# Kernel tuning notes

Hardware: AMD Instinct MI355X
Metric: run time of the kernel (lower is better)

## Reference

```python
import jax, jax.numpy as jnp
import numpy as np

B, C, D, L, CTX = 8, 320, 24, 77, 768
NUM_GROUPS = 32
EPS = 1e-5


def setup_inputs() -> dict:
    key = jax.random.key(0)
    ks = jax.random.split(key, 8)
    s = 0.02
    return {
        "x": jax.random.normal(ks[0], (B, C, D, D, D), jnp.float32),
        "context": jax.random.normal(ks[1], (B, L, CTX), jnp.float32),
        "Wq": jax.random.normal(ks[2], (C, C), jnp.float32) * s,
        "bq": jnp.zeros((C,), jnp.float32),
        "Wk": jax.random.normal(ks[3], (C, CTX), jnp.float32) * s,
        "bk": jnp.zeros((C,), jnp.float32),
        "Wv": jax.random.normal(ks[4], (C, CTX), jnp.float32) * s,
        "bv": jnp.zeros((C,), jnp.float32),
        "Wo": jax.random.normal(ks[5], (C, C), jnp.float32) * s,
        "bo": jnp.zeros((C,), jnp.float32),
        "gamma": jnp.ones((C,), jnp.float32),
        "beta": jnp.zeros((C,), jnp.float32),
    }


def reference(x, context, Wq, bq, Wk, bk, Wv, bv, Wo, bo, gamma, beta):
    b, c = x.shape[:2]
    spatial = x.shape[2:]
    xf = x.reshape(b, c, -1)                                # [B, C, N]
    # 1x1 Conv3d == per-position channel matmul
    q = jnp.einsum('oc,bcn->bon', Wq, xf) + bq[None, :, None]
    ctx_t = context.transpose(0, 2, 1)                      # [B, CTX, L]
    k = jnp.einsum('oc,bcl->bol', Wk, ctx_t) + bk[None, :, None]
    v = jnp.einsum('oc,bcl->bol', Wv, ctx_t) + bv[None, :, None]
    # scores [B, N, L], scaled by C^-0.5 (int(C) in the original)
    qk = jnp.einsum('bcn,bcl->bnl', q, k) * (float(c) ** -0.5)
    w = jax.nn.softmax(qk, axis=-1)
    h = jnp.einsum('bcl,bnl->bcn', v, w)                    # [B, C, N]
    h = jnp.einsum('oc,bcn->bon', Wo, h) + bo[None, :, None]
    xr = h + xf                                             # residual
    # GroupNorm over (C/G, spatial) per group
    g = NUM_GROUPS
    xg = xr.reshape(b, g, -1)
    mu = jnp.mean(xg, axis=-1, keepdims=True)
    var = jnp.var(xg, axis=-1, keepdims=True)
    xn = ((xg - mu) * jax.lax.rsqrt(var + EPS)).reshape(b, c, -1)
    xn = xn * gamma[None, :, None] + beta[None, :, None]
    out = xn * jax.nn.sigmoid(xn)                           # Swish
    return out.reshape(b, c, *spatial)
```

## Files before the change

### kernel.cpp

```cpp
#include <hip/hip_runtime.h>
#include <hip/hip_bf16.h>

#define B_ 8
#define C_ 320
#define N_ 13824
#define L_ 77
#define LP 80
#define LV 96
#define CTXD 768
#define CPG 10
#define EPS_ 1e-5f
#define SCALE_ 0.05590169943749474f
#define TROW 656

typedef __attribute__((__ext_vector_type__(4))) float f32x4;
typedef __attribute__((__ext_vector_type__(8))) short s16x8;

#define WS_ACCUM 0
#define WS_T     2048
#define WS_KST   4608
#define WS_VST   414208
#define WS_K2F   823808
#define WS_V2F   1233408
#define WS_WQT   1724928
#define WS_WO    1929728

__device__ __forceinline__ unsigned short f2bf(float f) {
  union { float f; unsigned u; } v; v.f = f;
  unsigned r = v.u + 0x7FFFu + ((v.u >> 16) & 1u);
  return (unsigned short)(r >> 16);
}
__device__ __forceinline__ float bf2f(unsigned short s) {
  union { unsigned u; float f; } v; v.u = ((unsigned)s) << 16;
  return v.f;
}
__device__ __forceinline__ s16x8 cvt8(const float* p) {
  f32x4 a = *reinterpret_cast<const f32x4*>(p);
  f32x4 b = *reinterpret_cast<const f32x4*>(p + 4);
  s16x8 r;
  r[0] = (short)f2bf(a[0]); r[1] = (short)f2bf(a[1]);
  r[2] = (short)f2bf(a[2]); r[3] = (short)f2bf(a[3]);
  r[4] = (short)f2bf(b[0]); r[5] = (short)f2bf(b[1]);
  r[6] = (short)f2bf(b[2]); r[7] = (short)f2bf(b[3]);
  return r;
}
__device__ __forceinline__ f32x4 MFMA(s16x8 a, s16x8 b, f32x4 c) {
  return __builtin_amdgcn_mfma_f32_16x16x32_bf16(a, b, c, 0, 0, 0);
}

__global__ __launch_bounds__(256) void prep_kernel(const float* __restrict__ Wq,
                                                   const float* __restrict__ Wo,
                                                   const float* __restrict__ ctx,
                                                   const float* __restrict__ Wk,
                                                   const float* __restrict__ bk,
                                                   const float* __restrict__ Wv,
                                                   const float* __restrict__ bv,
                                                   unsigned short* __restrict__ wqT,
                                                   unsigned short* __restrict__ wo_bf,
                                                   unsigned short* __restrict__ kst,
                                                   unsigned short* __restrict__ vst,
                                                   float* __restrict__ zws) {
  int bid = blockIdx.x;
  if (bid < 400) {
    int t = bid * 256 + threadIdx.x;
    if (t >= C_ * C_) return;
    int o = t / C_, c = t - o * C_;
    wqT[c * C_ + o] = f2bf(Wq[t]);
    wo_bf[t] = f2bf(Wo[t]);
    return;
  }
  int kb = bid - 400;
  { int t = kb * 256 + threadIdx.x; if (t < 1152) zws[t] = 0.f; }
  int lt = kb % 5;
  int kb5 = kb / 5;
  int b = kb5 / 5;
  int oc = kb5 % 5;
  int w = threadIdx.x >> 6, lane = threadIdx.x & 63;
  int r = lane & 15, h = lane >> 4;
  int o_row = oc * 64 + w * 16 + r;
  int l = lt * 16 + r;
  bool lok = (l < L_);
  f32x4 ak = {}, av = {};
  for (int ks = 0; ks < 24; ++ks) {
    int c0 = ks * 32 + h * 8;
    s16x8 aWk = cvt8(Wk + o_row * CTXD + c0);
    s16x8 aWv = cvt8(Wv + o_row * CTXD + c0);
    s16x8 bfr = {0,0,0,0,0,0,0,0};
    if (lok) bfr = cvt8(ctx + (b * L_ + l) * CTXD + c0);
    ak = MFMA(aWk, bfr, ak);
    av = MFMA(aWv, bfr, av);
  }
#pragma unroll
  for (int j = 0; j < 4; ++j) {
    int o = oc * 64 + w * 16 + h * 4 + j;
    float bkv = bk[o], bvv = bv[o];
    unsigned short kw = lok ? f2bf(SCALE_ * (ak[j] + bkv)) : (unsigned short)0;
    unsigned short vw = lok ? f2bf(av[j] + bvv) : (unsigned short)0;
    kst[(b * LP + l) * C_ + o] = kw;
    vst[(b * LP + l) * C_ + o] = vw;
  }
}

__global__ __launch_bounds__(256) void kv2_kernel(const unsigned short* __restrict__ wqT,
                                                  const unsigned short* __restrict__ wo_bf,
                                                  const unsigned short* __restrict__ kst,
                                                  const unsigned short* __restrict__ vst,
                                                  const float* __restrict__ bq,
                                                  float* __restrict__ tbuf,
                                                  unsigned short* __restrict__ k2F,
                                                  unsigned short* __restrict__ v2F) {
  int b = blockIdx.x / 5;
  int cc = blockIdx.x % 5;
  int w = threadIdx.x >> 6, lane = threadIdx.x & 63;
  int r = lane & 15, h = lane >> 4;
  int c_row = cc * 64 + w * 16 + r;
  f32x4 a2[5] = {}, av[5] = {};
#pragma unroll
  for (int ks = 0; ks < 10; ++ks) {
    int o0 = ks * 32 + h * 8;
    s16x8 aq = *reinterpret_cast<const s16x8*>(wqT + c_row * C_ + o0);
    s16x8 ao = *reinterpret_cast<const s16x8*>(wo_bf + c_row * C_ + o0);
#pragma unroll
    for (int nt = 0; nt < 5; ++nt) {
      int l = nt * 16 + r;
      s16x8 bk_ = *reinterpret_cast<const s16x8*>(kst + (b * LP + l) * C_ + o0);
      s16x8 bv_ = *reinterpret_cast<const s16x8*>(vst + (b * LP + l) * C_ + o0);
      a2[nt] = MFMA(aq, bk_, a2[nt]);
      av[nt] = MFMA(ao, bv_, av[nt]);
    }
  }
#pragma unroll
  for (int j = 0; j < 4; ++j) {
    int c = cc * 64 + w * 16 + h * 4 + j;
    int ks2 = c >> 5, h2 = (c >> 3) & 3, j2 = c & 7;
    int cs = c / 80, mt = (c - cs * 80) >> 4, rc = c & 15;
#pragma unroll
    for (int nt = 0; nt < 5; ++nt) {
      int l = nt * 16 + r;
      k2F[(((b * 5 + nt) * 10 + ks2) << 9) + ((h2 * 16 + r) << 3) + j2] = f2bf(a2[nt][j]);
      int ksl = l >> 5, hl = (l >> 3) & 3, jl = l & 7;
      v2F[((((long)(b * 4 + cs) * 5 + mt) * 3 + ksl) << 9) + ((hl * 16 + rc) << 3) + jl]
          = f2bf(av[nt][j]);
    }
  }
  {
    int t = threadIdx.x;
    int m = cc * 4 + (t >> 6);
    int cs = m / 5, mt = m % 5;
    long base = (((long)(b * 4 + cs) * 5 + mt) * 3 + 2) << 9;
    *reinterpret_cast<unsigned long long*>(v2F + base + 256 + (t & 63) * 4) = 0ull;
  }
  if (cc == 0 && threadIdx.x < LP) {
    int l = threadIdx.x;
    float acc = 0.f;
    for (int o8 = 0; o8 < C_; o8 += 8) {
      s16x8 kv = *reinterpret_cast<const s16x8*>(kst + (b * LP + l) * C_ + o8);
#pragma unroll
      for (int j = 0; j < 8; ++j) acc += bq[o8 + j] * bf2f((unsigned short)kv[j]);
    }
    tbuf[b * LP + l] = acc;
  }
}

__global__ __launch_bounds__(256)
__attribute__((amdgpu_waves_per_eu(2, 3)))
void fused_kernel(const float* __restrict__ x,
                  const unsigned short* __restrict__ k2F,
                  const unsigned short* __restrict__ v2F,
                  const float* __restrict__ tbuf,
                  const float* __restrict__ bo,
                  float* __restrict__ accum,
                  float* __restrict__ hout) {
  __shared__ __align__(16) unsigned short tile[64][328];
  __shared__ __align__(16) char smem2[12288];
  unsigned short (*pw)[512] = (unsigned short (*)[512])smem2;
  float (*ch)[2] = (float (*)[2])smem2;
  char* tb = (char*)&tile[0][0];
  int bid = blockIdx.x;
  int b = bid & 7;
  int n0 = (bid >> 3) * 64;
  int tid = threadIdx.x;
  int w = tid >> 6, lane = tid & 63, r = lane & 15, h = lane >> 4;
  const unsigned short* k2f = k2F + ((long)b * 50 << 9);

  s16x8 kfA[5], kfB[5];
#pragma unroll
  for (int nt = 0; nt < 5; ++nt)
    kfA[nt] = *reinterpret_cast<const s16x8*>(k2f + ((nt * 10) << 9) + (lane << 3));

  {
    int s_ = tid & 15;
    int cp = tid >> 4;
    const float* xb = x + (long)b * C_ * N_ + n0 + s_ * 4;
    f32x4 va[10], vb[10];
#pragma unroll
    for (int it = 0; it < 10; ++it) {
      const float* p = xb + (long)(it * 32 + cp * 2) * N_;
      va[it] = *reinterpret_cast<const f32x4*>(p);
      vb[it] = *reinterpret_cast<const f32x4*>(p + N_);
    }
#pragma unroll
    for (int it = 0; it < 10; ++it) {
      int cbyte = (it * 32 + cp * 2) * 2;
#pragma unroll
      for (int q = 0; q < 4; ++q) {
        int row = s_ * 4 + q;
        unsigned pk = (unsigned)f2bf(va[it][q]) | ((unsigned)f2bf(vb[it][q]) << 16);
        *reinterpret_cast<unsigned*>(tb + row * TROW + (cbyte ^ (row & 48))) = pk;
      }
    }
  }
  *reinterpret_cast<unsigned long long*>(&pw[8 + (tid >> 6)][256 + (tid & 63) * 4]) = 0ull;
  __syncthreads();

  int arow = w * 16 + r;
  int abase = arow * TROW;
  int akey = arow & 48;
  f32x4 sacc[5] = {};
#define SCHUNK(KS, KC, KN)                                                      \
  {                                                                             \
    s16x8 a = *reinterpret_cast<const s16x8*>(                                  \
        tb + abase + (((KS * 32 + h * 8) * 2) ^ akey));                         \
    if (KS < 9) {                                                               \
      _Pragma("unroll") for (int nt = 0; nt < 5; ++nt)                          \
          KN[nt] = *reinterpret_cast<const s16x8*>(                             \
              k2f + ((nt * 10 + KS + 1) << 9) + (lane << 3));                   \
    }                                                                           \
    _Pragma("unroll") for (int nt = 0; nt < 5; ++nt)                            \
      sacc[nt] = MFMA(a, KC[nt], sacc[nt]);                                     \
  }
  SCHUNK(0, kfA, kfB) SCHUNK(1, kfB, kfA) SCHUNK(2, kfA, kfB)
  SCHUNK(3, kfB, kfA) SCHUNK(4, kfA, kfB) SCHUNK(5, kfB, kfA)
  SCHUNK(6, kfA, kfB) SCHUNK(7, kfB, kfA) SCHUNK(8, kfA, kfB)
  SCHUNK(9, kfB, kfA)
#undef SCHUNK

#pragma unroll
  for (int nt = 0; nt < 5; ++nt) {
    float tl = tbuf[b * LP + nt * 16 + r];
#pragma unroll
    for (int j = 0; j < 4; ++j) sacc[nt][j] += tl;
  }
  bool maskpad = (r >= 13);
#pragma unroll
  for (int j = 0; j < 4; ++j) {
    float m = -1e30f;
#pragma unroll
    for (int nt = 0; nt < 5; ++nt) {
      float v = (nt == 4 && maskpad) ? -1e30f : sacc[nt][j];
      m = fmaxf(m, v);
    }
    for (int d = 1; d < 16; d <<= 1) m = fmaxf(m, __shfl_xor(m, d));
    float e[5]; float sum = 0.f;
#pragma unroll
    for (int nt = 0; nt < 5; ++nt) {
      float v = (nt == 4 && maskpad) ? 0.f : __expf(sacc[nt][j] - m);
      e[nt] = v; sum += v;
    }
    for (int d = 1; d < 16; d <<= 1) sum += __shfl_xor(sum, d);
    float inv = 1.f / sum;
    int r2 = h * 4 + j;
#pragma unroll
    for (int nt = 0; nt < 5; ++nt) {
      int l = nt * 16 + r;
      int ks = l >> 5, h2 = (l >> 3) & 3, j2 = l & 7;
      pw[ks * 4 + w][((h2 * 16 + r2) << 3) + j2] = f2bf(e[nt] * inv);
    }
  }
  __syncthreads();

  const unsigned short* vf = v2F + (((long)(b * 4 + w) * 15) << 9);
  f32x4 acc[4][5] = {};
  s16x8 va = *reinterpret_cast<const s16x8*>(vf + (lane << 3));
#pragma unroll
  for (int ks = 0; ks < 3; ++ks) {
    s16x8 bf[4];
#pragma unroll
    for (int nt = 0; nt < 4; ++nt)
      bf[nt] = *reinterpret_cast<const s16x8*>(&pw[ks * 4 + nt][lane << 3]);
#pragma unroll
    for (int mt = 0; mt < 5; ++mt) {
      s16x8 vn;
      if (!(ks == 2 && mt == 4)) {
        int ks2 = (mt == 4) ? ks + 1 : ks;
        int mt2 = (mt == 4) ? 0 : mt + 1;
        vn = *reinterpret_cast<const s16x8*>(vf + ((mt2 * 3 + ks2) << 9) + (lane << 3));
      }
#pragma unroll
      for (int nt = 0; nt < 4; ++nt) acc[nt][mt] = MFMA(va, bf[nt], acc[nt][mt]);
      if (!(ks == 2 && mt == 4)) va = vn;
    }
  }
  __syncthreads();

#pragma unroll
  for (int mt = 0; mt < 5; ++mt) {
    int cb = w * 80 + mt * 16 + h * 4;
    int cbyte = cb * 2;
    float bov[4];
#pragma unroll
    for (int j = 0; j < 4; ++j) bov[j] = bo[cb + j];
    float sv[4] = {0.f, 0.f, 0.f, 0.f}, sq[4] = {0.f, 0.f, 0.f, 0.f};
#pragma unroll
    for (int nt = 0; nt < 4; ++nt) {
      int n = nt * 16 + r;
      unsigned long long xr4 = *reinterpret_cast<const unsigned long long*>(
          tb + n * TROW + (cbyte ^ (n & 48)));
#pragma unroll
      for (int j = 0; j < 4; ++j) {
        float val = acc[nt][mt][j] + bov[j] + bf2f((unsigned short)(xr4 >> (j * 16)));
        long e = ((long)b * C_ + cb + j) * N_ + n0 + n;
        *reinterpret_cast<unsigned short*>(
            (char*)hout + ((e >> 11) << 13) + ((e & 2047) << 1)) = f2bf(val);
        sv[j] += val; sq[j] += val * val;
      }
    }
#pragma unroll
    for (int j = 0; j < 4; ++j) {
      for (int d = 1; d < 16; d <<= 1) {
        sv[j] += __shfl_xor(sv[j], d);
        sq[j] += __shfl_xor(sq[j], d);
      }
      if (r == 0) { ch[cb + j][0] = sv[j]; ch[cb + j][1] = sq[j]; }
    }
  }
  __syncthreads();
  if (tid < 32) {
    float s0 = 0.f, s1 = 0.f;
#pragma unroll
    for (int i = 0; i < CPG; ++i) { s0 += ch[tid * CPG + i][0]; s1 += ch[tid * CPG + i][1]; }
    atomicAdd(&accum[b * 64 + tid * 2], s0);
    atomicAdd(&accum[b * 64 + tid * 2 + 1], s1);
  }
}

__global__ __launch_bounds__(256) void norm_kernel(float* __restrict__ hout,
                                                   const float* __restrict__ accum,
                                                   const float* __restrict__ gamma,
                                                   const float* __restrict__ beta) {
  long idx0 = (long)blockIdx.x * 2048;
  int t = threadIdx.x;
  s16x8 hv = *reinterpret_cast<const s16x8*>((const char*)hout + idx0 * 4 + t * 16);
  __syncthreads();
  long idx = idx0 + (long)t * 8;
  int b = (int)(idx / ((long)C_ * N_));
  long rem = idx - (long)b * C_ * N_;
  int c = (int)(rem / N_);
  int g = c / CPG;
  float s0 = accum[b * 64 + g * 2], s1 = accum[b * 64 + g * 2 + 1];
  const float invc = 1.f / 138240.f;
  float mu = s0 * invc;
  float var = s1 * invc - mu * mu;
  float rstd = rsqrtf(var + EPS_);
  float ga = gamma[c], be = beta[c];
  f32x4 v0, v1;
#pragma unroll
  for (int q = 0; q < 4; ++q) {
    float y = (bf2f((unsigned short)hv[q]) - mu) * rstd * ga + be;
    v0[q] = y / (1.f + __expf(-y));
    float z = (bf2f((unsigned short)hv[q + 4]) - mu) * rstd * ga + be;
    v1[q] = z / (1.f + __expf(-z));
  }
  __builtin_nontemporal_store(v0, reinterpret_cast<f32x4*>(hout + idx));
  __builtin_nontemporal_store(v1, reinterpret_cast<f32x4*>(hout + idx + 4));
}

extern "C" void kernel_launch(void* const* d_in, const int* in_sizes, int n_in,
                              void* d_out, int out_size, void* d_ws, size_t ws_size,
                              hipStream_t stream) {
  const float* x     = (const float*)d_in[0];
  const float* ctx   = (const float*)d_in[1];
  const float* Wq    = (const float*)d_in[2];
  const float* bq    = (const float*)d_in[3];
  const float* Wk    = (const float*)d_in[4];
  const float* bk    = (const float*)d_in[5];
  const float* Wv    = (const float*)d_in[6];
  const float* bv    = (const float*)d_in[7];
  const float* Wo    = (const float*)d_in[8];
  const float* bo    = (const float*)d_in[9];
  const float* gamma = (const float*)d_in[10];
  const float* beta  = (const float*)d_in[11];
  float* out = (float*)d_out;
  char* ws = (char*)d_ws;

  float* accum = (float*)(ws + WS_ACCUM);
  float* tbuf  = (float*)(ws + WS_T);
  unsigned short* kst  = (unsigned short*)(ws + WS_KST);
  unsigned short* vst  = (unsigned short*)(ws + WS_VST);
  unsigned short* k2F  = (unsigned short*)(ws + WS_K2F);
  unsigned short* v2F  = (unsigned short*)(ws + WS_V2F);
  unsigned short* wqT  = (unsigned short*)(ws + WS_WQT);
  unsigned short* wo_b = (unsigned short*)(ws + WS_WO);

  prep_kernel<<<dim3(600), dim3(256), 0, stream>>>(Wq, Wo, ctx, Wk, bk, Wv, bv,
                                                   wqT, wo_b, kst, vst, (float*)ws);
  kv2_kernel<<<dim3(40), dim3(256), 0, stream>>>(wqT, wo_b, kst, vst, bq, tbuf, k2F, v2F);
  fused_kernel<<<dim3(1728), dim3(256), 0, stream>>>(x, k2F, v2F, tbuf, bo, accum, out);
  norm_kernel<<<dim3(17280), dim3(256), 0, stream>>>(out, accum, gamma, beta);
}
```

Measured before the change: 171.1 us.

## Process two spatial tiles per block and prefetch next x tile during compute

```diff
diff --git a/kernel.cpp b/kernel.cpp
--- a/kernel.cpp
+++ b/kernel.cpp
@@ -178,36 +178,37 @@
   char* tb = (char*)&tile[0][0];
   int bid = blockIdx.x;
   int b = bid & 7;
-  int n0 = (bid >> 3) * 64;
+  int n0base = (bid >> 3) * 128;
   int tid = threadIdx.x;
   int w = tid >> 6, lane = tid & 63, r = lane & 15, h = lane >> 4;
+  int s_ = tid & 15;
+  int cp = tid >> 4;
   const unsigned short* k2f = k2F + ((long)b * 50 << 9);
+  const float* xrowb = x + (long)b * C_ * N_;
 
   s16x8 kfA[5], kfB[5];
 #pragma unroll
   for (int nt = 0; nt < 5; ++nt)
     kfA[nt] = *reinterpret_cast<const s16x8*>(k2f + ((nt * 10) << 9) + (lane << 3));
 
+  f32x4 va[10], vb[10];
   {
-    int s_ = tid & 15;
-    int cp = tid >> 4;
-    const float* xb = x + (long)b * C_ * N_ + n0 + s_ * 4;
-    f32x4 va[10], vb[10];
+    const float* xb = xrowb + n0base + s_ * 4;
 #pragma unroll
     for (int it = 0; it < 10; ++it) {
       const float* p = xb + (long)(it * 32 + cp * 2) * N_;
       va[it] = *reinterpret_cast<const f32x4*>(p);
       vb[it] = *reinterpret_cast<const f32x4*>(p + N_);
     }
-#pragma unroll
-    for (int it = 0; it < 10; ++it) {
-      int cbyte = (it * 32 + cp * 2) * 2;
-#pragma unroll
-      for (int q = 0; q < 4; ++q) {
-        int row = s_ * 4 + q;
-        unsigned pk = (unsigned)f2bf(va[it][q]) | ((unsigned)f2bf(vb[it][q]) << 16);
-        *reinterpret_cast<unsigned*>(tb + row * TROW + (cbyte ^ (row & 48))) = pk;
-      }
+  }
+#pragma unroll
+  for (int it = 0; it < 10; ++it) {
+    int cbyte = (it * 32 + cp * 2) * 2;
+#pragma unroll
+    for (int q = 0; q < 4; ++q) {
+      int row = s_ * 4 + q;
+      unsigned pk = (unsigned)f2bf(va[it][q]) | ((unsigned)f2bf(vb[it][q]) << 16);
+      *reinterpret_cast<unsigned*>(tb + row * TROW + (cbyte ^ (row & 48))) = pk;
     }
   }
   *reinterpret_cast<unsigned long long*>(&pw[8 + (tid >> 6)][256 + (tid & 63) * 4]) = 0ull;
@@ -216,121 +217,153 @@
   int arow = w * 16 + r;
   int abase = arow * TROW;
   int akey = arow & 48;
-  f32x4 sacc[5] = {};
+
+#pragma unroll 1
+  for (int tt = 0; tt < 2; ++tt) {
+    int n0 = n0base + tt * 64;
+    f32x4 sacc[5] = {};
 #define SCHUNK(KS, KC, KN)                                                      \
-  {                                                                             \
-    s16x8 a = *reinterpret_cast<const s16x8*>(                                  \
-        tb + abase + (((KS * 32 + h * 8) * 2) ^ akey));                         \
-    if (KS < 9) {                                                               \
+    {                                                                           \
+      s16x8 a = *reinterpret_cast<const s16x8*>(                                \
+          tb + abase + (((KS * 32 + h * 8) * 2) ^ akey));                       \
+      if (KS < 9) {                                                             \
+        _Pragma("unroll") for (int nt = 0; nt < 5; ++nt)                        \
+            KN[nt] = *reinterpret_cast<const s16x8*>(                           \
+                k2f + ((nt * 10 + KS + 1) << 9) + (lane << 3));                 \
+      }                                                                         \
       _Pragma("unroll") for (int nt = 0; nt < 5; ++nt)                          \
-          KN[nt] = *reinterpret_cast<const s16x8*>(                             \
-              k2f + ((nt * 10 + KS + 1) << 9) + (lane << 3));                   \
-    }                                                                           \
-    _Pragma("unroll") for (int nt = 0; nt < 5; ++nt)                            \
-      sacc[nt] = MFMA(a, KC[nt], sacc[nt]);                                     \
-  }
-  SCHUNK(0, kfA, kfB) SCHUNK(1, kfB, kfA) SCHUNK(2, kfA, kfB)
-  SCHUNK(3, kfB, kfA) SCHUNK(4, kfA, kfB) SCHUNK(5, kfB, kfA)
-  SCHUNK(6, kfA, kfB) SCHUNK(7, kfB, kfA) SCHUNK(8, kfA, kfB)
-  SCHUNK(9, kfB, kfA)
+        sacc[nt] = MFMA(a, KC[nt], sacc[nt]);                                   \
+    }
+    SCHUNK(0, kfA, kfB) SCHUNK(1, kfB, kfA) SCHUNK(2, kfA, kfB)
+    SCHUNK(3, kfB, kfA) SCHUNK(4, kfA, kfB) SCHUNK(5, kfB, kfA)
+    SCHUNK(6, kfA, kfB) SCHUNK(7, kfB, kfA) SCHUNK(8, kfA, kfB)
+    SCHUNK(9, kfB, kfA)
 #undef SCHUNK
 
-#pragma unroll
-  for (int nt = 0; nt < 5; ++nt) {
-    float tl = tbuf[b * LP + nt * 16 + r];
-#pragma unroll
-    for (int j = 0; j < 4; ++j) sacc[nt][j] += tl;
-  }
-  bool maskpad = (r >= 13);
-#pragma unroll
-  for (int j = 0; j < 4; ++j) {
-    float m = -1e30f;
+    if (tt == 0) {
+      const float* xb = xrowb + n0base + 64 + s_ * 4;
+#pragma unroll
+      for (int it = 0; it < 10; ++it) {
+        const float* p = xb + (long)(it * 32 + cp * 2) * N_;
+        va[it] = *reinterpret_cast<const f32x4*>(p);
+        vb[it] = *reinterpret_cast<const f32x4*>(p + N_);
+      }
+    }
+
 #pragma unroll
     for (int nt = 0; nt < 5; ++nt) {
-      float v = (nt == 4 && maskpad) ? -1e30f : sacc[nt][j];
-      m = fmaxf(m, v);
-    }
-    for (int d = 1; d < 16; d <<= 1) m = fmaxf(m, __shfl_xor(m, d));
-    float e[5]; float sum = 0.f;
-#pragma unroll
-    for (int nt = 0; nt < 5; ++nt) {
-      float v = (nt == 4 && maskpad) ? 0.f : __expf(sacc[nt][j] - m);
-      e[nt] = v; sum += v;
-    }
-    for (int d = 1; d < 16; d <<= 1) sum += __shfl_xor(sum, d);
-    float inv = 1.f / sum;
-    int r2 = h * 4 + j;
-#pragma unroll
-    for (int nt = 0; nt < 5; ++nt) {
-      int l = nt * 16 + r;
-      int ks = l >> 5, h2 = (l >> 3) & 3, j2 = l & 7;
-      pw[ks * 4 + w][((h2 * 16 + r2) << 3) + j2] = f2bf(e[nt] * inv);
-    }
-  }
-  __syncthreads();
-
-  const unsigned short* vf = v2F + (((long)(b * 4 + w) * 15) << 9);
-  f32x4 acc[4][5] = {};
-  s16x8 va = *reinterpret_cast<const s16x8*>(vf + (lane << 3));
-#pragma unroll
-  for (int ks = 0; ks < 3; ++ks) {
-    s16x8 bf[4];
-#pragma unroll
-    for (int nt = 0; nt < 4; ++nt)
-      bf[nt] = *reinterpret_cast<const s16x8*>(&pw[ks * 4 + nt][lane << 3]);
+      float tl = tbuf[b * LP + nt * 16 + r];
+#pragma unroll
+      for (int j = 0; j < 4; ++j) sacc[nt][j] += tl;
+    }
+    bool maskpad = (r >= 13);
+#pragma unroll
+    for (int j = 0; j < 4; ++j) {
+      float m = -1e30f;
+#pragma unroll
+      for (int nt = 0; nt < 5; ++nt) {
+        float v = (nt == 4 && maskpad) ? -1e30f : sacc[nt][j];
+        m = fmaxf(m, v);
+      }
+      for (int d = 1; d < 16; d <<= 1) m = fmaxf(m, __shfl_xor(m, d));
+      float e[5]; float sum = 0.f;
+#pragma unroll
+      for (int nt = 0; nt < 5; ++nt) {
+        float v = (nt == 4 && maskpad) ? 0.f : __expf(sacc[nt][j] - m);
+        e[nt] = v; sum += v;
+      }
+      for (int d = 1; d < 16; d <<= 1) sum += __shfl_xor(sum, d);
+      float inv = 1.f / sum;
+      int r2 = h * 4 + j;
+#pragma unroll
+      for (int nt = 0; nt < 5; ++nt) {
+        int l = nt * 16 + r;
+        int ks = l >> 5, h2 = (l >> 3) & 3, j2 = l & 7;
+        pw[ks * 4 + w][((h2 * 16 + r2) << 3) + j2] = f2bf(e[nt] * inv);
+      }
+    }
+    __syncthreads();
+
+    const unsigned short* vf = v2F + (((long)(b * 4 + w) * 15) << 9);
+    f32x4 acc[4][5] = {};
+    s16x8 vfrag = *reinterpret_cast<const s16x8*>(vf + (lane << 3));
+#pragma unroll
+    for (int ks = 0; ks < 3; ++ks) {
+      s16x8 bf[4];
+#pragma unroll
+      for (int nt = 0; nt < 4; ++nt)
+        bf[nt] = *reinterpret_cast<const s16x8*>(&pw[ks * 4 + nt][lane << 3]);
+#pragma unroll
+      for (int mt = 0; mt < 5; ++mt) {
+        s16x8 vn;
+        if (!(ks == 2 && mt == 4)) {
+          int ks2 = (mt == 4) ? ks + 1 : ks;
+          int mt2 = (mt == 4) ? 0 : mt + 1;
+          vn = *reinterpret_cast<const s16x8*>(vf + ((mt2 * 3 + ks2) << 9) + (lane << 3));
+        }
+#pragma unroll
+        for (int nt = 0; nt < 4; ++nt) acc[nt][mt] = MFMA(vfrag, bf[nt], acc[nt][mt]);
+        if (!(ks == 2 && mt == 4)) vfrag = vn;
+      }
+    }
+    __syncthreads();
+
 #pragma unroll
     for (int mt = 0; mt < 5; ++mt) {
-      s16x8 vn;
-      if (!(ks == 2 && mt == 4)) {
-        int ks2 = (mt == 4) ? ks + 1 : ks;
-        int mt2 = (mt == 4) ? 0 : mt + 1;
-        vn = *reinterpret_cast<const s16x8*>(vf + ((mt2 * 3 + ks2) << 9) + (lane << 3));
-      }
-#pragma unroll
-      for (int nt = 0; nt < 4; ++nt) acc[nt][mt] = MFMA(va, bf[nt], acc[nt][mt]);
-      if (!(ks == 2 && mt == 4)) va = vn;
-    }
-  }
-  __syncthreads();
-
-#pragma unroll
-  for (int mt = 0; mt < 5; ++mt) {
-    int cb = w * 80 + mt * 16 + h * 4;
-    int cbyte = cb * 2;
-    float bov[4];
-#pragma unroll
-    for (int j = 0; j < 4; ++j) bov[j] = bo[cb + j];
-    float sv[4] = {0.f, 0.f, 0.f, 0.f}, sq[4] = {0.f, 0.f, 0.f, 0.f};
-#pragma unroll
-    for (int nt = 0; nt < 4; ++nt) {
-      int n = nt * 16 + r;
-      unsigned long long xr4 = *reinterpret_cast<const unsigned long long*>(
-          tb + n * TROW + (cbyte ^ (n & 48)));
+      int cb = w * 80 + mt * 16 + h * 4;
+      int cbyte = cb * 2;
+      float bov[4];
+#pragma unroll
+      for (int j = 0; j < 4; ++j) bov[j] = bo[cb + j];
+      float sv[4] = {0.f, 0.f, 0.f, 0.f}, sq[4] = {0.f, 0.f, 0.f, 0.f};
+#pragma unroll
+      for (int nt = 0; nt < 4; ++nt) {
+        int n = nt * 16 + r;
+        unsigned long long xr4 = *reinterpret_cast<const unsigned long long*>(
+            tb + n * TROW + (cbyte ^ (n & 48)));
+#pragma unroll
+        for (int j = 0; j < 4; ++j) {
+          float val = acc[nt][mt][j] + bov[j] + bf2f((unsigned short)(xr4 >> (j * 16)));
+          long e = ((long)b * C_ + cb + j) * N_ + n0 + n;
+          *reinterpret_cast<unsigned short*>(
+              (char*)hout + ((e >> 11) << 13) + ((e & 2047) << 1)) = f2bf(val);
+          sv[j] += val; sq[j] += val * val;
+        }
+      }
 #pragma unroll
       for (int j = 0; j < 4; ++j) {
-        float val = acc[nt][mt][j] + bov[j] + bf2f((unsigned short)(xr4 >> (j * 16)));
-        long e = ((long)b * C_ + cb + j) * N_ + n0 + n;
-        *reinterpret_cast<unsigned short*>(
-            (char*)hout + ((e >> 11) << 13) + ((e & 2047) << 1)) = f2bf(val);
-        sv[j] += val; sq[j] += val * val;
-      }
-    }
-#pragma unroll
-    for (int j = 0; j < 4; ++j) {
-      for (int d = 1; d < 16; d <<= 1) {
-        sv[j] += __shfl_xor(sv[j], d);
-        sq[j] += __shfl_xor(sq[j], d);
-      }
-      if (r == 0) { ch[cb + j][0] = sv[j]; ch[cb + j][1] = sq[j]; }
-    }
-  }
-  __syncthreads();
-  if (tid < 32) {
-    float s0 = 0.f, s1 = 0.f;
-#pragma unroll
-    for (int i = 0; i < CPG; ++i) { s0 += ch[tid * CPG + i][0]; s1 += ch[tid * CPG + i][1]; }
-    atomicAdd(&accum[b * 64 + tid * 2], s0);
-    atomicAdd(&accum[b * 64 + tid * 2 + 1], s1);
+        for (int d = 1; d < 16; d <<= 1) {
+          sv[j] += __shfl_xor(sv[j], d);
+          sq[j] += __shfl_xor(sq[j], d);
+        }
+        if (r == 0) { ch[cb + j][0] = sv[j]; ch[cb + j][1] = sq[j]; }
+      }
+    }
+    __syncthreads();
+    if (tid < 32) {
+      float s0 = 0.f, s1 = 0.f;
+#pragma unroll
+      for (int i = 0; i < CPG; ++i) { s0 += ch[tid * CPG + i][0]; s1 += ch[tid * CPG + i][1]; }
+      atomicAdd(&accum[b * 64 + tid * 2], s0);
+      atomicAdd(&accum[b * 64 + tid * 2 + 1], s1);
+    }
+    if (tt == 0) {
+      __syncthreads();
+#pragma unroll
+      for (int it = 0; it < 10; ++it) {
+        int cbyte = (it * 32 + cp * 2) * 2;
+#pragma unroll
+        for (int q = 0; q < 4; ++q) {
+          int row = s_ * 4 + q;
+          unsigned pk = (unsigned)f2bf(va[it][q]) | ((unsigned)f2bf(vb[it][q]) << 16);
+          *reinterpret_cast<unsigned*>(tb + row * TROW + (cbyte ^ (row & 48))) = pk;
+        }
+      }
+#pragma unroll
+      for (int nt = 0; nt < 5; ++nt)
+        kfA[nt] = *reinterpret_cast<const s16x8*>(k2f + ((nt * 10) << 9) + (lane << 3));
+      __syncthreads();
+    }
   }
 }
 
@@ -395,6 +428,6 @@
   prep_kernel<<<dim3(600), dim3(256), 0, stream>>>(Wq, Wo, ctx, Wk, bk, Wv, bv,
                                                    wqT, wo_b, kst, vst, (float*)ws);
   kv2_kernel<<<dim3(40), dim3(256), 0, stream>>>(wqT, wo_b, kst, vst, bq, tbuf, k2F, v2F);
-  fused_kernel<<<dim3(1728), dim3(256), 0, stream>>>(x, k2F, v2F, tbuf, bo, accum, out);
+  fused_kernel<<<dim3(864), dim3(256), 0, stream>>>(x, k2F, v2F, tbuf, bo, accum, out);
   norm_kernel<<<dim3(17280), dim3(256), 0, stream>>>(out, accum, gamma, beta);
 }
```

Result: slower. 459.0 us (+168.2%).
